# Optimization experiments

Hardware: AMD Instinct MI355X
Metric: run time of the kernel (lower is better)

Reference implementation:

```python
import jax, jax.numpy as jnp
import numpy as np

# ---- static configuration (mirrors C4WithSyscalls __init__/_build_keys) ----
MEM = 16384            # memory_size
OUT = 64               # output_size
NCTX = MEM + 5 + OUT   # context: [memory, PC, SP, BP, AX, OUT_LEN, output]
SCALE = 10.0
GATE_SCALE = 20.0
ADDR_BITS = int(np.ceil(np.log2(NCTX)))   # 15
TYPE_BITS = 5
KDIM = ADDR_BITS + TYPE_BITS
POWERS = jnp.asarray(2 ** np.arange(ADDR_BITS), jnp.int32)

# opcode values for the 15 experts: IMM,LEA,ADD,SUB,MUL,DIV,MOD,SHL,SHR,EQ,NE,LT,GT,LE,GE
OP_VALS = jnp.asarray([1., 2., 9., 10., 11., 12., 13., 14., 15., 3., 4., 5., 6., 7., 8.], jnp.float32)
# binary ops (everything except IMM, LEA) pop the stack: sp += 8
POP_MASK = jnp.asarray([0., 0.] + [1.] * 13, jnp.float32)


def _build_keys():
    addrs = np.arange(NCTX)
    bits = (addrs[:, None] // (2 ** np.arange(ADDR_BITS))) % 2
    addr_keys = (2.0 * bits - 1.0) * SCALE                       # [N, ADDR_BITS]
    type_tags = np.full((NCTX, TYPE_BITS), -SCALE)
    type_tags[MEM, 0] = SCALE      # PC
    type_tags[MEM + 1, 1] = SCALE  # SP
    type_tags[MEM + 2, 2] = SCALE  # BP
    type_tags[MEM + 3, 3] = SCALE  # AX
    type_tags[MEM + 4:, 4] = SCALE  # OUT_LEN + output slots
    return jnp.asarray(np.concatenate([addr_keys, type_tags], 1), jnp.float32)

KEYS = _build_keys()  # [NCTX, KDIM]


def silu_threshold(x, scale=GATE_SCALE):
    d = scale * x
    return (jax.nn.silu(d + 0.5 * scale) - jax.nn.silu(d - 0.5 * scale)) / scale


def eq_gate(a, b, scale=GATE_SCALE):
    diff = a - b
    return silu_threshold(diff + 0.5, scale) * silu_threshold(-diff + 0.5, scale)


def attend(context, addr):
    """Soft-addressed gather: context [B,NCTX], addr [B] float -> (value [B], weights [B,NCTX])."""
    ai = jnp.clip(addr, 0.0, float(NCTX - 1)).astype(jnp.int32)
    bits = (ai[:, None] // POWERS) % 2
    addr_q = (2.0 * bits.astype(jnp.float32) - 1.0) * SCALE                 # [B, ADDR_BITS]
    type_q = jnp.full((addr.shape[0], TYPE_BITS), -SCALE, jnp.float32)      # memory_type tag
    q = jnp.concatenate([addr_q, type_q], axis=1)                           # [B, KDIM]
    scores = jnp.einsum('nd,bd->bn', KEYS, q) / np.sqrt(KDIM)
    w = jax.nn.softmax(scores, axis=1)
    return jnp.einsum('bn,bn->b', w, context), w


def expert_outputs(a, b, imm, bp):
    """a = stack_top, b = ax. Returns [B, 15] new-ax candidates per expert."""
    safeb = jnp.where(jnp.abs(b) < 1e-6, 1e-6, b)
    div = a / safeb
    mod = a - safeb * jnp.floor(div)
    sh = jnp.clip(b, 0.0, 31.0)
    eq = eq_gate(a, b)
    lt = jax.nn.sigmoid(GATE_SCALE * (b - a - 0.5))
    gt = jax.nn.sigmoid(GATE_SCALE * (a - b - 0.5))
    return jnp.stack([
        imm,               # IMM
        bp + imm,          # LEA
        a + b,             # ADD
        a - b,             # SUB
        a * b,             # MUL
        div,               # DIV
        mod,               # MOD
        a * jnp.exp2(sh),  # SHL
        a * jnp.exp2(-sh), # SHR
        eq,                # EQ
        1.0 - eq,          # NE
        lt,                # LT
        gt,                # GT
        1.0 - gt,          # LE
        1.0 - lt,          # GE
    ], axis=-1)


def _forward(memory, output, ax, pc, sp, bp, out_len, num_steps):
    B = memory.shape[0]
    pcf, spf, bpf = pc.astype(jnp.float32), sp.astype(jnp.float32), bp.astype(jnp.float32)
    olf = out_len.astype(jnp.float32)[:, None]

    def step(carry, _):
        pc_, sp_, bp_, ax_, mem_ = carry
        regs = jnp.stack([pc_, sp_, bp_, ax_], axis=1)                    # [B,4]
        context = jnp.concatenate([mem_, regs, olf, output], axis=1)     # [B,NCTX]
        inst, _ = attend(context, pc_)
        imm = jnp.floor(inst / 256.0)
        opcode = inst - imm * 256.0
        stack_top, w_sp = attend(context, sp_)
        gates = eq_gate(opcode[:, None], OP_VALS[None, :])                # [B,15] soft top-1
        outs = expert_outputs(stack_top, ax_, imm, bp_)                   # [B,15]
        gsum = gates.sum(-1)
        new_ax = (gates * outs).sum(-1) + (1.0 - gsum) * ax_              # NoOp default
        pop_g = (gates * POP_MASK).sum(-1)
        new_sp = sp_ + 8.0 * pop_g
        new_pc = pc_ + 8.0
        # soft scatter: write new_ax back at the (soft) stack-top address
        new_mem = mem_ + pop_g[:, None] * w_sp[:, :MEM] * (new_ax[:, None] - mem_)
        return (new_pc, new_sp, bp_, new_ax, new_mem), None

    carry, _ = jax.lax.scan(step, (pcf, spf, bpf, ax, memory), None, length=num_steps)
    return carry[4]  # final memory [B, MEM]


def setup_inputs() -> dict:
    key = jax.random.key(0)
    k = jax.random.split(key, 8)
    B = 1024
    return {
        'memory': jax.random.normal(k[0], (B, MEM), jnp.float32),
        'output': jax.random.normal(k[1], (B, OUT), jnp.float32),
        'ax': jax.random.normal(k[2], (B,), jnp.float32),
        'pc': jax.random.randint(k[3], (B,), 0, MEM, jnp.int32),
        'sp': jax.random.randint(k[4], (B,), 0, MEM, jnp.int32),
        'bp': jax.random.randint(k[5], (B,), 0, MEM, jnp.int32),
        'out_len': jax.random.randint(k[6], (B,), 0, OUT, jnp.int32),
        'num_steps': 16,
    }


def reference(memory, output, ax, pc, sp, bp, out_len, num_steps):
    return _forward(memory, output, ax, pc, sp, bp, out_len, num_steps)
```

## Files before the change

### kernel.cpp

```cpp
#include <hip/hip_runtime.h>
#include <math.h>

#define MEMSZ 16384
#define NCTX  16453

typedef float f4 __attribute__((ext_vector_type(4)));

__device__ __forceinline__ float sigmoidf_(float x) {
    return __builtin_amdgcn_rcpf(1.0f + __expf(-x));
}
__device__ __forceinline__ float siluf_(float x) {
    return x * sigmoidf_(x);
}
__device__ __forceinline__ float silu_thr(float x) {
    float d = 20.0f * x;
    return (siluf_(d + 10.0f) - siluf_(d - 10.0f)) * 0.05f;
}
__device__ __forceinline__ float eq_gate_d(float diff) {
    return silu_thr(diff + 0.5f) * silu_thr(0.5f - diff);
}

__global__ __launch_bounds__(256) void copy_kernel(const f4* __restrict__ src,
                                                   f4* __restrict__ dst, int n4) {
    int i = blockIdx.x * blockDim.x + threadIdx.x;
    if (i < n4)
        __builtin_nontemporal_store(__builtin_nontemporal_load(&src[i]), &dst[i]);
}

__global__ __launch_bounds__(64) void sim_kernel(
        float* __restrict__ mem,
        const float* __restrict__ outp,
        const float* __restrict__ ax_in,
        const int* __restrict__ pc_in,
        const int* __restrict__ sp_in,
        const int* __restrict__ bp_in,
        const int* __restrict__ ol_in,
        const int* __restrict__ nstep,
        int B) {
    int b = blockIdx.x * 64 + threadIdx.x;
    if (b >= B) return;

    float* __restrict__ mrow = mem + (size_t)b * MEMSZ;
    const float* __restrict__ orow = outp + (size_t)b * 64;

    float pc  = (float)pc_in[b];
    float sp  = (float)sp_in[b];
    float bp  = (float)bp_in[b];
    float ax  = ax_in[b];
    float olf = (float)ol_in[b];
    int   T   = nstep[0];

    const float opv[15] = {1.f, 2.f, 9.f, 10.f, 11.f, 12.f, 13.f, 14.f, 15.f,
                           3.f, 4.f, 5.f, 6.f, 7.f, 8.f};

    for (int t = 0; t < T; ++t) {
        float a1 = fminf(fmaxf(pc, 0.0f), (float)(NCTX - 1));
        int   ai = (int)a1;
        float a2 = fminf(fmaxf(sp, 0.0f), (float)(NCTX - 1));
        int   si = (int)a2;
        int pidx   = (ai < MEMSZ) ? ai : (ai - MEMSZ);
        int target = (si < MEMSZ) ? si : (si - MEMSZ);
        float m_pc = mrow[pidx];
        float mtv  = mrow[target];

        float inst;
        if (ai < MEMSZ) {
            inst = m_pc;
        } else {
            int r = ai - MEMSZ;
            float cv = (r == 0) ? pc
                     : (r == 1) ? sp
                     : (r == 2) ? bp
                     : (r == 3) ? ax
                     : (r == 4) ? olf
                                : orow[r - 5];
            inst = 0.5f * (cv + m_pc);
        }
        float imm = floorf(inst * (1.0f / 256.0f));
        float opc = inst - imm * 256.0f;

        float stv, wfac;
        if (si < MEMSZ) {
            stv = mtv;
            wfac = 1.0f;
        } else {
            int r = si - MEMSZ;
            float cv = (r == 0) ? pc
                     : (r == 1) ? sp
                     : (r == 2) ? bp
                     : (r == 3) ? ax
                     : (r == 4) ? olf
                                : orow[r - 5];
            stv = 0.5f * (cv + mtv);
            wfac = 0.5f;
        }

        float a = stv, bv = ax;
        float safeb = (fabsf(bv) < 1e-6f) ? 1e-6f : bv;
        float dvv = a / safeb;
        float md  = a - safeb * floorf(dvv);
        float sh  = fminf(fmaxf(bv, 0.0f), 31.0f);
        float eq  = eq_gate_d(a - bv);
        float lt  = sigmoidf_(20.0f * (bv - a - 0.5f));
        float gt  = sigmoidf_(20.0f * (a - bv - 0.5f));
        float outs[15] = {
            imm,
            bp + imm,
            a + bv,
            a - bv,
            a * bv,
            dvv,
            md,
            a * exp2f(sh),
            a * exp2f(-sh),
            eq,
            1.0f - eq,
            lt,
            gt,
            1.0f - gt,
            1.0f - lt
        };

        float gsum = 0.0f, acc = 0.0f, pop = 0.0f;
#pragma unroll
        for (int j = 0; j < 15; ++j) {
            float g = eq_gate_d(opc - opv[j]);
            gsum += g;
            acc  += g * outs[j];
            if (j >= 2) pop += g;
        }
        float nax = acc + (1.0f - gsum) * ax;

        mrow[target] = mtv + pop * wfac * (nax - mtv);

        sp = sp + 8.0f * pop;
        pc = pc + 8.0f;
        ax = nax;
    }
}

extern "C" void kernel_launch(void* const* d_in, const int* in_sizes, int n_in,
                              void* d_out, int out_size, void* d_ws, size_t ws_size,
                              hipStream_t stream) {
    const float* memory = (const float*)d_in[0];
    const float* output = (const float*)d_in[1];
    const float* ax     = (const float*)d_in[2];
    const int*   pc     = (const int*)d_in[3];
    const int*   sp     = (const int*)d_in[4];
    const int*   bp     = (const int*)d_in[5];
    const int*   ol     = (const int*)d_in[6];
    const int*   ns     = (const int*)d_in[7];

    int B = in_sizes[0] / MEMSZ;
    int n4 = (B * MEMSZ) / 4;

    hipLaunchKernelGGL(copy_kernel, dim3((n4 + 255) / 256), dim3(256), 0, stream,
                       (const f4*)memory, (f4*)d_out, n4);
    hipLaunchKernelGGL(sim_kernel, dim3((B + 63) / 64), dim3(64), 0, stream,
                       (float*)d_out, output, ax, pc, sp, bp, ol, ns, B);
}
```

Measured before the change: 158.2 us.

## Prefetch all PC reads and next stack read with store-forwarding for T=16

```diff
diff --git a/kernel.cpp b/kernel.cpp
--- a/kernel.cpp
+++ b/kernel.cpp
@@ -43,7 +43,7 @@
     float* __restrict__ mrow = mem + (size_t)b * MEMSZ;
     const float* __restrict__ orow = outp + (size_t)b * 64;
 
-    float pc  = (float)pc_in[b];
+    float pc0 = (float)pc_in[b];
     float sp  = (float)sp_in[b];
     float bp  = (float)bp_in[b];
     float ax  = ax_in[b];
@@ -53,89 +53,198 @@
     const float opv[15] = {1.f, 2.f, 9.f, 10.f, 11.f, 12.f, 13.f, 14.f, 15.f,
                            3.f, 4.f, 5.f, 6.f, 7.f, 8.f};
 
-    for (int t = 0; t < T; ++t) {
-        float a1 = fminf(fmaxf(pc, 0.0f), (float)(NCTX - 1));
-        int   ai = (int)a1;
+    if (T == 16) {
+        float pf[16];
+        int   pfi[16];
+#pragma unroll
+        for (int t = 0; t < 16; ++t) {
+            float pcr = pc0 + 8.0f * (float)t;
+            float a1 = fminf(fmaxf(pcr, 0.0f), (float)(NCTX - 1));
+            int ai = (int)a1;
+            pfi[t] = ai;
+            int pidx = (ai < MEMSZ) ? ai : ai - MEMSZ;
+            pf[t] = mrow[pidx];
+        }
+
+        int   sidx[16];
+        float sval[16];
+#pragma unroll
+        for (int j = 0; j < 16; ++j) { sidx[j] = -1; sval[j] = 0.0f; }
+
         float a2 = fminf(fmaxf(sp, 0.0f), (float)(NCTX - 1));
-        int   si = (int)a2;
-        int pidx   = (ai < MEMSZ) ? ai : (ai - MEMSZ);
-        int target = (si < MEMSZ) ? si : (si - MEMSZ);
-        float m_pc = mrow[pidx];
-        float mtv  = mrow[target];
-
-        float inst;
-        if (ai < MEMSZ) {
-            inst = m_pc;
-        } else {
-            int r = ai - MEMSZ;
-            float cv = (r == 0) ? pc
-                     : (r == 1) ? sp
-                     : (r == 2) ? bp
-                     : (r == 3) ? ax
-                     : (r == 4) ? olf
-                                : orow[r - 5];
-            inst = 0.5f * (cv + m_pc);
+        int   si  = (int)a2;
+        int   tgt = (si < MEMSZ) ? si : si - MEMSZ;
+        float raw = mrow[tgt];
+
+#pragma unroll
+        for (int t = 0; t < 16; ++t) {
+            float pcr = pc0 + 8.0f * (float)t;
+
+            int ai   = pfi[t];
+            int pidx = (ai < MEMSZ) ? ai : ai - MEMSZ;
+            float m_pc = pf[t];
+#pragma unroll
+            for (int j = 0; j < 16; ++j)
+                if (j < t && sidx[j] == pidx) m_pc = sval[j];
+
+            float inst;
+            if (ai < MEMSZ) {
+                inst = m_pc;
+            } else {
+                int r = ai - MEMSZ;
+                float cv = (r == 0) ? pcr
+                         : (r == 1) ? sp
+                         : (r == 2) ? bp
+                         : (r == 3) ? ax
+                         : (r == 4) ? olf
+                                    : orow[r - 5];
+                inst = 0.5f * (cv + m_pc);
+            }
+            float imm = floorf(inst * (1.0f / 256.0f));
+            float opc = inst - imm * 256.0f;
+
+            float g[15];
+#pragma unroll
+            for (int j = 0; j < 15; ++j) g[j] = eq_gate_d(opc - opv[j]);
+            float gsum = 0.0f;
+#pragma unroll
+            for (int j = 0; j < 15; ++j) gsum += g[j];
+            float pop = 0.0f;
+#pragma unroll
+            for (int j = 2; j < 15; ++j) pop += g[j];
+
+            float sp_next = sp + 8.0f * pop;
+            int   si_n = 0, tgt_n = 0;
+            float raw_n = 0.0f;
+            if (t < 15) {
+                float a2n = fminf(fmaxf(sp_next, 0.0f), (float)(NCTX - 1));
+                si_n  = (int)a2n;
+                tgt_n = (si_n < MEMSZ) ? si_n : si_n - MEMSZ;
+                raw_n = mrow[tgt_n];
+            }
+
+            float mtv = raw;
+#pragma unroll
+            for (int j = 0; j < 16; ++j)
+                if (j < t && sidx[j] == tgt) mtv = sval[j];
+
+            float stv, wfac;
+            if (si < MEMSZ) {
+                stv = mtv;
+                wfac = 1.0f;
+            } else {
+                int r = si - MEMSZ;
+                float cv = (r == 0) ? pcr
+                         : (r == 1) ? sp
+                         : (r == 2) ? bp
+                         : (r == 3) ? ax
+                         : (r == 4) ? olf
+                                    : orow[r - 5];
+                stv = 0.5f * (cv + mtv);
+                wfac = 0.5f;
+            }
+
+            float a = stv, bv = ax;
+            float safeb = (fabsf(bv) < 1e-6f) ? 1e-6f : bv;
+            float dvv = a / safeb;
+            float md  = a - safeb * floorf(dvv);
+            float sh  = fminf(fmaxf(bv, 0.0f), 31.0f);
+            float eqg = eq_gate_d(a - bv);
+            float lt  = sigmoidf_(20.0f * (bv - a - 0.5f));
+            float gt  = sigmoidf_(20.0f * (a - bv - 0.5f));
+            float outs[15] = {
+                imm, bp + imm, a + bv, a - bv, a * bv, dvv, md,
+                a * exp2f(sh), a * exp2f(-sh),
+                eqg, 1.0f - eqg, lt, gt, 1.0f - gt, 1.0f - lt
+            };
+            float acc = 0.0f;
+#pragma unroll
+            for (int j = 0; j < 15; ++j) acc += g[j] * outs[j];
+            float nax = acc + (1.0f - gsum) * ax;
+
+            float vnew = mtv + pop * wfac * (nax - mtv);
+            mrow[tgt] = vnew;
+            sidx[t] = tgt;
+            sval[t] = vnew;
+
+            sp = sp_next;
+            ax = nax;
+            if (t < 15) { si = si_n; tgt = tgt_n; raw = raw_n; }
         }
-        float imm = floorf(inst * (1.0f / 256.0f));
-        float opc = inst - imm * 256.0f;
-
-        float stv, wfac;
-        if (si < MEMSZ) {
-            stv = mtv;
-            wfac = 1.0f;
-        } else {
-            int r = si - MEMSZ;
-            float cv = (r == 0) ? pc
-                     : (r == 1) ? sp
-                     : (r == 2) ? bp
-                     : (r == 3) ? ax
-                     : (r == 4) ? olf
-                                : orow[r - 5];
-            stv = 0.5f * (cv + mtv);
-            wfac = 0.5f;
+    } else {
+        float pc = pc0;
+        for (int t = 0; t < T; ++t) {
+            float a1 = fminf(fmaxf(pc, 0.0f), (float)(NCTX - 1));
+            int   ai = (int)a1;
+            float a2 = fminf(fmaxf(sp, 0.0f), (float)(NCTX - 1));
+            int   si = (int)a2;
+            int pidx   = (ai < MEMSZ) ? ai : (ai - MEMSZ);
+            int target = (si < MEMSZ) ? si : (si - MEMSZ);
+            float m_pc = mrow[pidx];
+            float mtv  = mrow[target];
+
+            float inst;
+            if (ai < MEMSZ) {
+                inst = m_pc;
+            } else {
+                int r = ai - MEMSZ;
+                float cv = (r == 0) ? pc
+                         : (r == 1) ? sp
+                         : (r == 2) ? bp
+                         : (r == 3) ? ax
+                         : (r == 4) ? olf
+                                    : orow[r - 5];
+                inst = 0.5f * (cv + m_pc);
+            }
+            float imm = floorf(inst * (1.0f / 256.0f));
+            float opc = inst - imm * 256.0f;
+
+            float stv, wfac;
+            if (si < MEMSZ) {
+                stv = mtv;
+                wfac = 1.0f;
+            } else {
+                int r = si - MEMSZ;
+                float cv = (r == 0) ? pc
+                         : (r == 1) ? sp
+                         : (r == 2) ? bp
+                         : (r == 3) ? ax
+                         : (r == 4) ? olf
+                                    : orow[r - 5];
+                stv = 0.5f * (cv + mtv);
+                wfac = 0.5f;
+            }
+
+            float a = stv, bv = ax;
+            float safeb = (fabsf(bv) < 1e-6f) ? 1e-6f : bv;
+            float dvv = a / safeb;
+            float md  = a - safeb * floorf(dvv);
+            float sh  = fminf(fmaxf(bv, 0.0f), 31.0f);
+            float eqg = eq_gate_d(a - bv);
+            float lt  = sigmoidf_(20.0f * (bv - a - 0.5f));
+            float gt  = sigmoidf_(20.0f * (a - bv - 0.5f));
+            float outs[15] = {
+                imm, bp + imm, a + bv, a - bv, a * bv, dvv, md,
+                a * exp2f(sh), a * exp2f(-sh),
+                eqg, 1.0f - eqg, lt, gt, 1.0f - gt, 1.0f - lt
+            };
+
+            float gsum = 0.0f, acc = 0.0f, pop = 0.0f;
+#pragma unroll
+            for (int j = 0; j < 15; ++j) {
+                float gg = eq_gate_d(opc - opv[j]);
+                gsum += gg;
+                acc  += gg * outs[j];
+                if (j >= 2) pop += gg;
+            }
+            float nax = acc + (1.0f - gsum) * ax;
+
+            mrow[target] = mtv + pop * wfac * (nax - mtv);
+
+            sp = sp + 8.0f * pop;
+            pc = pc + 8.0f;
+            ax = nax;
         }
-
-        float a = stv, bv = ax;
-        float safeb = (fabsf(bv) < 1e-6f) ? 1e-6f : bv;
-        float dvv = a / safeb;
-        float md  = a - safeb * floorf(dvv);
-        float sh  = fminf(fmaxf(bv, 0.0f), 31.0f);
-        float eq  = eq_gate_d(a - bv);
-        float lt  = sigmoidf_(20.0f * (bv - a - 0.5f));
-        float gt  = sigmoidf_(20.0f * (a - bv - 0.5f));
-        float outs[15] = {
-            imm,
-            bp + imm,
-            a + bv,
-            a - bv,
-            a * bv,
-            dvv,
-            md,
-            a * exp2f(sh),
-            a * exp2f(-sh),
-            eq,
-            1.0f - eq,
-            lt,
-            gt,
-            1.0f - gt,
-            1.0f - lt
-        };
-
-        float gsum = 0.0f, acc = 0.0f, pop = 0.0f;
-#pragma unroll
-        for (int j = 0; j < 15; ++j) {
-            float g = eq_gate_d(opc - opv[j]);
-            gsum += g;
-            acc  += g * outs[j];
-            if (j >= 2) pop += g;
-        }
-        float nax = acc + (1.0f - gsum) * ax;
-
-        mrow[target] = mtv + pop * wfac * (nax - mtv);
-
-        sp = sp + 8.0f * pop;
-        pc = pc + 8.0f;
-        ax = nax;
     }
 }
 
```

Result: no change. 156.4 us (-1.1%).
